# Optimization experiments

Measured on AMD Instinct MI355X. Metric: run time of the kernel, lower is better.

The kernel has to match this reference:

```python
import jax, jax.numpy as jnp
import numpy as np

K = 40  # k_point

def lrelu(v):
    return jax.nn.leaky_relu(v, 0.2)

def graph_feature(x, k):
    # x: [B, C, N] -> edge features [B, 2C, N, k] = concat(x_j - x_i, x_i)
    xx = jnp.sum(x * x, axis=1)                          # [B,N]
    inner = jnp.einsum('bcn,bcm->bnm', x, x)             # [B,N,N]
    dist = 2.0 * inner - xx[:, :, None] - xx[:, None, :] # negative squared distance
    idx = jax.lax.top_k(dist, k)[1]                      # [B,N,k] nearest neighbors
    xt = jnp.transpose(x, (0, 2, 1))                     # [B,N,C]
    nbr = jax.vmap(lambda f, i: f[i])(xt, idx)           # [B,N,k,C] gather
    ctr = xt[:, :, None, :]
    feat = jnp.concatenate([nbr - ctr, jnp.broadcast_to(ctr, nbr.shape)], axis=-1)
    return jnp.transpose(feat, (0, 3, 1, 2))             # [B,2C,N,k]

def conv2(f, w):  # 1x1 conv2d, no bias
    return jnp.einsum('bcnk,oc->bonk', f, w)

def conv1(f, w):  # 1x1 conv1d, no bias
    return jnp.einsum('bcn,oc->bon', f, w)

def edge_block(x, ws, k):
    f = graph_feature(x, k)
    for w in ws:
        f = lrelu(conv2(f, w))
    return jnp.max(f, axis=-1)                           # max over k neighbors

def setup_inputs() -> dict:
    key = jax.random.key(0)
    ks = jax.random.split(key, 20)
    B, N, NCLS, NSEG, D = 8, 2048, 16, 50, 1024
    def w(kk, o, c, s=0.05):
        return jax.random.normal(kk, (o, c), jnp.float32) * s
    return {
        'x': jax.random.normal(ks[0], (B, 3, N), jnp.float32),
        'l': jax.random.uniform(ks[1], (B, NCLS), dtype=jnp.float32),
        't_c1': w(ks[2], 64, 6), 't_c2': w(ks[3], 128, 64), 't_c3': w(ks[4], 1024, 128),
        't_f1': w(ks[5], 512, 1024), 't_f2': w(ks[6], 256, 512),
        't_f3_w': w(ks[7], 9, 256, 0.01),
        't_f3_b': jnp.eye(3, dtype=jnp.float32).reshape(9),  # identity-transform init
        'b1a': w(ks[8], 64, 6), 'b1b': w(ks[9], 64, 64),
        'b2a': w(ks[10], 64, 128), 'b2b': w(ks[11], 64, 64),
        'b3a': w(ks[12], 64, 128),
        'm1': w(ks[13], D, 192), 'm2': w(ks[14], 64, NCLS),
        'h1': w(ks[15], 256, D + 256), 'h2': w(ks[16], 256, 256),
        'h3': w(ks[17], 128, 256), 'h4': w(ks[18], NSEG, 128),
    }

def reference(x, l, t_c1, t_c2, t_c3, t_f1, t_f2, t_f3_w, t_f3_b,
              b1a, b1b, b2a, b2b, b3a, m1, m2, h1, h2, h3, h4):
    B, _, N = x.shape
    # transform net on graph features of raw points
    x0 = graph_feature(x, K)                              # [B,6,N,K]
    t = lrelu(conv2(x0, t_c1))
    t = lrelu(conv2(t, t_c2))
    t = jnp.max(t, axis=-1)                               # [B,128,N]
    t = lrelu(conv1(t, t_c3))
    t = jnp.max(t, axis=-1)                               # [B,1024]
    t = lrelu(t @ t_f1.T)
    t = lrelu(t @ t_f2.T)
    T = (t @ t_f3_w.T + t_f3_b).reshape(B, 3, 3)
    x = jnp.einsum('bji,bjn->bin', T, x)                  # T^T @ x
    # edge-conv blocks
    x1 = edge_block(x, [b1a, b1b], K)                     # [B,64,N]
    x2 = edge_block(x1, [b2a, b2b], K)                    # [B,64,N]
    x3 = edge_block(x2, [b3a], K)                         # [B,64,N]
    cat = jnp.concatenate([x1, x2, x3], axis=1)           # [B,192,N]
    g = jnp.max(lrelu(conv1(cat, m1)), axis=-1, keepdims=True)  # [B,1024,1]
    lv = lrelu(jnp.einsum('bc,oc->bo', l, m2))[:, :, None]      # [B,64,1]
    glob = jnp.broadcast_to(jnp.concatenate([g, lv], axis=1), (B, g.shape[1] + 64, N))
    h = jnp.concatenate([glob, x1, x2, x3], axis=1)       # [B,1280,N]
    h = lrelu(conv1(h, h1))
    h = lrelu(conv1(h, h2))
    h = lrelu(conv1(h, h3))
    return conv1(h, h4)                                   # [B,50,N]
```

## Files before the change

### kernel.cpp

```cpp
#include <hip/hip_runtime.h>
#include <cstdint>

#define NPTS 2048
#define BATCH 8
#define KNN 40

__device__ __forceinline__ float lrelu(float v){ return fmaxf(v, 0.2f*v); }
__device__ __forceinline__ bool better(float v1,int i1,float v2,int i2){
  return (v1>v2) || (v1==v2 && i1<i2);
}
__device__ __forceinline__ float4 ld4(const float* p){ return *(const float4*)p; }

#define INSERT8(v,id,d,m) \
  if (better(d, m, v[7], id[7])){ \
    v[7]=d; id[7]=m; \
    { if (better(v[7],id[7],v[6],id[6])){ float tv=v[6];int ti=id[6]; v[6]=v[7];id[6]=id[7]; v[7]=tv;id[7]=ti; } } \
    { if (better(v[6],id[6],v[5],id[5])){ float tv=v[5];int ti=id[5]; v[5]=v[6];id[5]=id[6]; v[6]=tv;id[6]=ti; } } \
    { if (better(v[5],id[5],v[4],id[4])){ float tv=v[4];int ti=id[4]; v[4]=v[5];id[4]=id[5]; v[5]=tv;id[5]=ti; } } \
    { if (better(v[4],id[4],v[3],id[3])){ float tv=v[3];int ti=id[3]; v[3]=v[4];id[3]=id[4]; v[4]=tv;id[4]=ti; } } \
    { if (better(v[3],id[3],v[2],id[2])){ float tv=v[2];int ti=id[2]; v[2]=v[3];id[2]=id[3]; v[3]=tv;id[3]=ti; } } \
    { if (better(v[2],id[2],v[1],id[1])){ float tv=v[1];int ti=id[1]; v[1]=v[2];id[1]=id[2]; v[2]=tv;id[2]=ti; } } \
    { if (better(v[1],id[1],v[0],id[0])){ float tv=v[0];int ti=id[0]; v[0]=v[1];id[0]=id[1]; v[1]=tv;id[1]=ti; } } \
  }

__global__ void transpose_kernel(const float* __restrict__ src, float* __restrict__ dst,
                                 int R, int C, int ld, int off){
  int i = blockIdx.x*256 + threadIdx.x;
  if (i < R*C){ int r = i / C, c = i % C; dst[c*R + r] = src[r*ld + off + c]; }
}

template<int TAG>
__global__ void norms_rows_kernel(const float* __restrict__ x, float* __restrict__ xx, int N){
  int b = blockIdx.y; int n = blockIdx.x*256 + threadIdx.x;
  const float* xb = x + (size_t)b*3*N;
  float v0 = xb[n], v1 = xb[N+n], v2 = xb[2*N+n];
  xx[(size_t)b*N + n] = v0*v0 + v1*v1 + v2*v2;
}

template<int TAG>
__global__ void norms_cl_kernel(const float* __restrict__ f, int off, float* __restrict__ xx, int N){
  int b = blockIdx.y; int n = blockIdx.x*256 + threadIdx.x;
  const float4* p = (const float4*)(f + ((size_t)b*N + n)*192 + off);
  float s = 0.f;
#pragma unroll
  for (int q=0;q<16;q++){ float4 v = p[q]; s += v.x*v.x + v.y*v.y + v.z*v.z + v.w*v.w; }
  xx[(size_t)b*N + n] = s;
}

__device__ __forceinline__ void sort8(float (&v)[8], int (&id)[8]){
#define CE(a,bq) { if (better(v[bq],id[bq],v[a],id[a])){ float tv=v[a]; int ti=id[a]; v[a]=v[bq]; id[a]=id[bq]; v[bq]=tv; id[bq]=ti; } }
  CE(0,1) CE(2,3) CE(4,5) CE(6,7)
  CE(0,2) CE(1,3) CE(4,6) CE(5,7)
  CE(1,2) CE(5,6)
  CE(0,4) CE(1,5) CE(2,6) CE(3,7)
  CE(2,4) CE(3,5)
  CE(1,2) CE(3,4) CE(5,6)
#undef CE
}

template<int TAG>
__global__ __launch_bounds__(256) void knn3_kernel(
    const float* __restrict__ xrows, const float* __restrict__ xx,
    int* __restrict__ idxT, int N){
  const int b = blockIdx.y, tid = threadIdx.x;
  const int w = tid>>6, lane = tid&63;
  const int nq = blockIdx.x*4 + w;
  const float* xb = xrows + (size_t)b*3*N;
  const float* xxb = xx + (size_t)b*N;
  float c0 = xb[nq], c1 = xb[N+nq], c2 = xb[2*N+nq];
  float xxn = xxb[nq];
  float v[8]; int id[8];
#pragma unroll
  for (int j=0;j<8;j++){ v[j]=-__builtin_inff(); id[j]=0x7FFFFFFF; }
  for (int j=0;j<32;j++){
    int m = j*64 + lane;
    float s = c0*xb[m] + c1*xb[N+m] + c2*xb[2*N+m];
    float d = 2.f*s - xxn - xxb[m];
    INSERT8(v, id, d, m)
  }
  float lastv = 0.f; int lasti = 0;
  int win = 0;
  for (int r=0;r<KNN;r++){
    float bv = v[0]; int bi = id[0];
#pragma unroll
    for (int off=32; off; off>>=1){
      float ov = __shfl_xor(bv, off);
      int   oi = __shfl_xor(bi, off);
      if (better(ov, oi, bv, bi)){ bv = ov; bi = oi; }
    }
    if (lane == r) win = bi;
    if (id[0] == bi){
      lastv = v[0]; lasti = id[0];
#pragma unroll
      for (int j=0;j<7;j++){ v[j]=v[j+1]; id[j]=id[j+1]; }
      v[7] = -__builtin_inff(); id[7] = 0x7FFFFFFF;
      if (id[0] == 0x7FFFFFFF){
        float nv = -__builtin_inff(); int ni = 0x7FFFFFFF;
        for (int j=0;j<32;j++){
          int m = j*64 + lane;
          float s = c0*xb[m] + c1*xb[N+m] + c2*xb[2*N+m];
          float dd = 2.f*s - xxn - xxb[m];
          if (better(lastv, lasti, dd, m) && better(dd, m, nv, ni)){ nv=dd; ni=m; }
        }
        v[0] = nv; id[0] = ni;
      }
    }
  }
  if (lane < KNN) idxT[((size_t)b*KNN + lane)*N + nq] = win;
}

template<int TAG>
__global__ __launch_bounds__(256) void knn64_kernel(
    const float* __restrict__ featT, int featOff,
    const float* __restrict__ xx, int* __restrict__ idxT, int N){
  const int b = blockIdx.y, tid = threadIdx.x;
  const int w = tid>>6, lane = tid&63;
  __shared__ float cand[32*64];
  __shared__ float dist[4*2048];
  const float* fb = featT + featOff;
  const float* xxb = xx + (size_t)b*N;
  const int nq = blockIdx.x*4 + w;
  const int h = lane>>5;
  float4 ctr8[8];
  {
    const float4* cp = (const float4*)(fb + ((size_t)b*N + nq)*192);
#pragma unroll
    for (int q=0;q<8;q++) ctr8[q] = cp[h*8 + q];
  }
  float xxn = xxb[nq];
  float* dw = &dist[w*2048];
  float4 g[2];
#pragma unroll
  for (int r=0;r<2;r++){
    int k2 = tid + 256*r;
    int c = k2>>4, f = k2&15;
    g[r] = ld4(&fb[((size_t)b*N + c)*192 + 4*f]);
  }
  const int cc = lane&31, swz = cc&15, qb = h*8;
  for (int t=0;t<64;t++){
    __syncthreads();
#pragma unroll
    for (int r=0;r<2;r++){
      int k2 = tid + 256*r;
      int c = k2>>4, f = k2&15;
      *(float4*)&cand[(c<<6) + ((f ^ (c&15))<<2)] = g[r];
    }
    __syncthreads();
    if (t+1 < 64){
      int m0n = (t+1)*32;
#pragma unroll
      for (int r=0;r<2;r++){
        int k2 = tid + 256*r;
        int c = k2>>4, f = k2&15;
        g[r] = ld4(&fb[((size_t)b*N + m0n + c)*192 + 4*f]);
      }
    }
    float s0=0.f,s1=0.f,s2=0.f,s3=0.f;
#pragma unroll
    for (int j=0;j<8;j++){
      float4 mv = *(const float4*)&cand[(cc<<6) + (((qb + j) ^ swz)<<2)];
      s0 = fmaf(ctr8[j].x, mv.x, s0);
      s1 = fmaf(ctr8[j].y, mv.y, s1);
      s2 = fmaf(ctr8[j].z, mv.z, s2);
      s3 = fmaf(ctr8[j].w, mv.w, s3);
    }
    float p = (s0+s1)+(s2+s3);
    float tot = p + __shfl_xor(p, 32);
    if (h == (t&1)){
      int m = t*32 + cc;
      dw[(t>>1)*64 + lane] = 2.f*tot - xxn - xxb[m];
    }
  }
  float v[8]; int id[8];
#pragma unroll
  for (int j=0;j<8;j++){ v[j]=dw[j*64+lane]; id[j]=j*64+lane; }
  sort8(v, id);
#pragma unroll
  for (int gq=1; gq<4; gq++){
    float a[8]; int ai[8];
#pragma unroll
    for (int j=0;j<8;j++){ a[j]=dw[(gq*8+j)*64+lane]; ai[j]=(gq*8+j)*64+lane; }
    sort8(a, ai);
    float m_[8]; int mi_[8];
#pragma unroll
    for (int k=0;k<8;k++){
      if (better(a[7-k], ai[7-k], v[k], id[k])){ m_[k]=a[7-k]; mi_[k]=ai[7-k]; }
      else                                     { m_[k]=v[k];   mi_[k]=id[k]; }
    }
#define CEB(x,y) { if (better(m_[y],mi_[y],m_[x],mi_[x])){ float tv=m_[x];int ti=mi_[x]; m_[x]=m_[y];mi_[x]=mi_[y]; m_[y]=tv;mi_[y]=ti; } }
    CEB(0,4) CEB(1,5) CEB(2,6) CEB(3,7)
    CEB(0,2) CEB(1,3) CEB(4,6) CEB(5,7)
    CEB(0,1) CEB(2,3) CEB(4,5) CEB(6,7)
#undef CEB
#pragma unroll
    for (int k=0;k<8;k++){ v[k]=m_[k]; id[k]=mi_[k]; }
  }
  float lastv = 0.f; int lasti = 0;
  int win = 0;
  for (int r=0;r<KNN;r++){
    float bv = v[0]; int bi = id[0];
#pragma unroll
    for (int off=32; off; off>>=1){
      float ov = __shfl_xor(bv, off);
      int   oi = __shfl_xor(bi, off);
      if (better(ov, oi, bv, bi)){ bv = ov; bi = oi; }
    }
    if (lane == r) win = bi;
    if (id[0] == bi){
      lastv = v[0]; lasti = id[0];
#pragma unroll
      for (int j=0;j<7;j++){ v[j]=v[j+1]; id[j]=id[j+1]; }
      v[7] = -__builtin_inff(); id[7] = 0x7FFFFFFF;
      if (id[0] == 0x7FFFFFFF){
        float nv = -__builtin_inff(); int ni = 0x7FFFFFFF;
        for (int j=0;j<32;j++){
          float vv = dw[j*64 + lane]; int m = j*64 + lane;
          if (better(lastv, lasti, vv, m) && better(vv, m, nv, ni)){ nv=vv; ni=m; }
        }
        v[0] = nv; id[0] = ni;
      }
    }
  }
  if (lane < KNN) idxT[((size_t)b*KNN + lane)*N + nq] = win;
}


__global__ __launch_bounds__(256) void edgeA_kernel(
    const float* __restrict__ x, const int* __restrict__ idxT,
    const float* __restrict__ w1, const float* __restrict__ w2,
    float* __restrict__ tT, int N){
  __shared__ float w1aT[3*64];
  __shared__ float wd3T[3*64];
  __shared__ float w2T[64*128];
  __shared__ float aT3[4][3*16];
  __shared__ float s1T[4][64*16];
  const int tid = threadIdx.x, w = tid>>6, lane = tid&63;
  const int oq = lane&7, rg = lane>>3;
  const int o0 = oq*8, r0 = rg*2;
  const int b = blockIdx.y, n0 = blockIdx.x*16;
  for (int i=tid; i<192; i+=256){
    int o = i&63, c = i/64;
    float a = w1[o*6+c];
    w1aT[c*64+o] = a; wd3T[c*64+o] = w1[o*6+3+c] - a;
  }
  for (int i=tid; i<128*64; i+=256){
    int o = i>>6, c = i&63;
    w2T[c*128+o] = w2[o*64+c];
  }
  if (tid < 48){ int c = tid>>4, r = tid&15; aT3[0][c*16+r] = x[((size_t)b*3+c)*N + n0 + r]; }
  __syncthreads();
  float base[16];
#pragma unroll
  for (int i=0;i<16;i++) base[i]=0.f;
#pragma unroll
  for (int c=0;c<3;c++){
    float4 wA = ld4(&wd3T[c*64+o0]), wB = ld4(&wd3T[c*64+o0+4]);
    float2 av = *(const float2*)&aT3[0][c*16+r0];
    float wv[8] = {wA.x,wA.y,wA.z,wA.w,wB.x,wB.y,wB.z,wB.w};
    float rv[2] = {av.x,av.y};
#pragma unroll
    for (int oo=0;oo<8;oo++)
#pragma unroll
      for (int rr=0;rr<2;rr++) base[oo*2+rr] = fmaf(wv[oo], rv[rr], base[oo*2+rr]);
  }
  __syncthreads();
  float mx[32];
#pragma unroll
  for (int i=0;i<32;i++) mx[i] = -__builtin_inff();
  for (int it=0; it<10; it++){
    int k = it*4 + w;
    int m = idxT[((size_t)b*KNN + k)*N + n0 + (lane&15)];
    if (lane < 48){ int c = lane>>4; aT3[w][c*16 + (lane&15)] = x[((size_t)b*3+c)*N + m]; }
    float acc[16];
#pragma unroll
    for (int i=0;i<16;i++) acc[i] = base[i];
#pragma unroll
    for (int c=0;c<3;c++){
      float4 wA = ld4(&w1aT[c*64+o0]), wB = ld4(&w1aT[c*64+o0+4]);
      float2 av = *(const float2*)&aT3[w][c*16+r0];
      float wv[8] = {wA.x,wA.y,wA.z,wA.w,wB.x,wB.y,wB.z,wB.w};
      float rv[2] = {av.x,av.y};
#pragma unroll
      for (int oo=0;oo<8;oo++)
#pragma unroll
        for (int rr=0;rr<2;rr++) acc[oo*2+rr] = fmaf(wv[oo], rv[rr], acc[oo*2+rr]);
    }
#pragma unroll
    for (int oo=0;oo<8;oo++){
      float2 sv; sv.x = lrelu(acc[oo*2]); sv.y = lrelu(acc[oo*2+1]);
      *(float2*)&s1T[w][(o0+oo)*16 + r0] = sv;
    }
    float acc2[32];
#pragma unroll
    for (int i=0;i<32;i++) acc2[i]=0.f;
    for (int c=0;c<64;c++){
      float2 av = *(const float2*)&s1T[w][c*16 + r0];
#pragma unroll
      for (int p=0;p<4;p++){
        float4 wv = ld4(&w2T[c*128 + p*32 + oq*4]);
        acc2[p*8+0] = fmaf(wv.x, av.x, acc2[p*8+0]);
        acc2[p*8+1] = fmaf(wv.x, av.y, acc2[p*8+1]);
        acc2[p*8+2] = fmaf(wv.y, av.x, acc2[p*8+2]);
        acc2[p*8+3] = fmaf(wv.y, av.y, acc2[p*8+3]);
        acc2[p*8+4] = fmaf(wv.z, av.x, acc2[p*8+4]);
        acc2[p*8+5] = fmaf(wv.z, av.y, acc2[p*8+5]);
        acc2[p*8+6] = fmaf(wv.w, av.x, acc2[p*8+6]);
        acc2[p*8+7] = fmaf(wv.w, av.y, acc2[p*8+7]);
      }
    }
#pragma unroll
    for (int i=0;i<32;i++) mx[i] = fmaxf(mx[i], lrelu(acc2[i]));
  }
  __syncthreads();
#pragma unroll
  for (int rr=0;rr<2;rr++){
#pragma unroll
    for (int p=0;p<4;p++){
      float4 a = make_float4(mx[p*8+0+rr], mx[p*8+2+rr], mx[p*8+4+rr], mx[p*8+6+rr]);
      *(float4*)&w2T[w*2048 + (r0+rr)*128 + p*32 + oq*4] = a;
    }
  }
  __syncthreads();
  for (int i=tid; i<2048; i+=256){
    float vv = fmaxf(fmaxf(w2T[i], w2T[2048+i]), fmaxf(w2T[4096+i], w2T[6144+i]));
    int r = i>>7, o = i&127;
    tT[((size_t)b*N + n0 + r)*128 + o] = vv;
  }
}

__global__ __launch_bounds__(128) void edgeB_kernel(
    const float* __restrict__ xp, const int* __restrict__ idxT,
    const float* __restrict__ w1, const float* __restrict__ w2,
    float* __restrict__ catT, int N){
  __shared__ float w1aT[3*64];
  __shared__ float wd3T[3*64];
  __shared__ float w2T[64*64];
  __shared__ float aT3[2][3*32];
  __shared__ float s1T[2][64*32];
  const int tid = threadIdx.x, w = tid>>6, lane = tid&63;
  const int oq = lane&7, rg = lane>>3;
  const int o0 = oq*8, r0 = rg*4;
  const int b = blockIdx.y, n0 = blockIdx.x*32;
  for (int i=tid; i<192; i+=128){
    int o = i&63, c = i>>6;
    float a = w1[o*6+c], bb = w1[o*6+3+c];
    w1aT[c*64+o] = a; wd3T[c*64+o] = bb - a;
  }
  for (int i=tid; i<64*64; i+=128){
    int o = i>>6, c = i&63;
    w2T[c*64+o] = w2[o*64+c];
  }
  if (tid < 32){
#pragma unroll
    for (int c=0;c<3;c++) aT3[0][c*32+tid] = xp[((size_t)b*3+c)*N + n0 + tid];
  }
  __syncthreads();
  float base[32];
#pragma unroll
  for (int i=0;i<32;i++) base[i]=0.f;
#pragma unroll
  for (int c=0;c<3;c++){
    float4 w0 = ld4(&wd3T[c*64+o0]), w1v = ld4(&wd3T[c*64+o0+4]);
    float4 av = ld4(&aT3[0][c*32+r0]);
    float wv[8] = {w0.x,w0.y,w0.z,w0.w,w1v.x,w1v.y,w1v.z,w1v.w};
    float rv[4] = {av.x,av.y,av.z,av.w};
#pragma unroll
    for (int oo=0;oo<8;oo++)
#pragma unroll
      for (int rr=0;rr<4;rr++) base[oo*4+rr] = fmaf(wv[oo], rv[rr], base[oo*4+rr]);
  }
  __syncthreads();
  float mx[32];
#pragma unroll
  for (int i=0;i<32;i++) mx[i] = -__builtin_inff();
  for (int it=0; it<20; it++){
    int k = it*2 + w;
    {
      int row = lane&31;
      int m = idxT[((size_t)b*KNN + k)*N + n0 + row];
      if (lane < 32){
#pragma unroll
        for (int c=0;c<3;c++) aT3[w][c*32+row] = xp[((size_t)b*3+c)*N + m];
      }
    }
    float acc[32];
#pragma unroll
    for (int i=0;i<32;i++) acc[i] = base[i];
#pragma unroll
    for (int c=0;c<3;c++){
      float4 w0 = ld4(&w1aT[c*64+o0]), w1v = ld4(&w1aT[c*64+o0+4]);
      float4 av = ld4(&aT3[w][c*32+r0]);
      float wv[8] = {w0.x,w0.y,w0.z,w0.w,w1v.x,w1v.y,w1v.z,w1v.w};
      float rv[4] = {av.x,av.y,av.z,av.w};
#pragma unroll
      for (int oo=0;oo<8;oo++)
#pragma unroll
        for (int rr=0;rr<4;rr++) acc[oo*4+rr] = fmaf(wv[oo], rv[rr], acc[oo*4+rr]);
    }
#pragma unroll
    for (int oo=0;oo<8;oo++){
      float4 sv = make_float4(lrelu(acc[oo*4+0]), lrelu(acc[oo*4+1]), lrelu(acc[oo*4+2]), lrelu(acc[oo*4+3]));
      *(float4*)&s1T[w][(o0+oo)*32 + r0] = sv;
    }
    float acc2[32];
#pragma unroll
    for (int i=0;i<32;i++) acc2[i]=0.f;
    for (int c=0;c<64;c++){
      float4 w0 = ld4(&w2T[c*64+o0]), w1v = ld4(&w2T[c*64+o0+4]);
      float4 av = ld4(&s1T[w][c*32+r0]);
      float wv[8] = {w0.x,w0.y,w0.z,w0.w,w1v.x,w1v.y,w1v.z,w1v.w};
      float rv[4] = {av.x,av.y,av.z,av.w};
#pragma unroll
      for (int oo=0;oo<8;oo++)
#pragma unroll
        for (int rr=0;rr<4;rr++) acc2[oo*4+rr] = fmaf(wv[oo], rv[rr], acc2[oo*4+rr]);
    }
#pragma unroll
    for (int i=0;i<32;i++) mx[i] = fmaxf(mx[i], lrelu(acc2[i]));
  }
  __syncthreads();
#pragma unroll
  for (int rr=0;rr<4;rr++){
    float4 a = make_float4(mx[0*4+rr], mx[1*4+rr], mx[2*4+rr], mx[3*4+rr]);
    float4 bq = make_float4(mx[4*4+rr], mx[5*4+rr], mx[6*4+rr], mx[7*4+rr]);
    *(float4*)&s1T[w][(r0+rr)*64 + o0] = a;
    *(float4*)&s1T[w][(r0+rr)*64 + o0 + 4] = bq;
  }
  __syncthreads();
  for (int i=tid; i<2048; i+=128){
    float v = fmaxf(s1T[0][i], s1T[1][i]);
    int r = i>>6, o = i&63;
    catT[((size_t)b*N + n0 + r)*192 + o] = v;
  }
}

__global__ __launch_bounds__(128) void edgeC_kernel(
    const float* __restrict__ inT, int inOff, const int* __restrict__ idxT,
    const float* __restrict__ w1, const float* __restrict__ w2,
    float* __restrict__ catT, int outOff, int N){
  __shared__ float w1T[64*64];
  __shared__ float w2T[64*64];
  __shared__ float aT[2][64*32];
  __shared__ float s1T[2][64*32];
  const int tid = threadIdx.x, w = tid>>6, lane = tid&63;
  const int oq = lane&7, rg = lane>>3;
  const int o0 = oq*8, r0 = rg*4;
  const int b = blockIdx.y, n0 = blockIdx.x*32;
  for (int i=tid; i<64*64; i+=128){
    int o = i>>6, c = i&63;
    float a = w1[o*128+c], bb = w1[o*128+64+c];
    w1T[c*64+o] = a; w2T[c*64+o] = bb - a;
  }
  for (int i=tid; i<512; i+=128){
    int p = i>>4, cq = i&15;
    float4 v = ld4(&inT[((size_t)b*N + n0 + p)*192 + inOff + cq*4]);
    aT[0][(cq*4+0)*32+p] = v.x; aT[0][(cq*4+1)*32+p] = v.y;
    aT[0][(cq*4+2)*32+p] = v.z; aT[0][(cq*4+3)*32+p] = v.w;
  }
  __syncthreads();
  float base[32];
#pragma unroll
  for (int i=0;i<32;i++) base[i]=0.f;
  for (int c=0;c<64;c++){
    float4 w0 = ld4(&w2T[c*64+o0]), w1v = ld4(&w2T[c*64+o0+4]);
    float4 av = ld4(&aT[0][c*32+r0]);
    float wv[8] = {w0.x,w0.y,w0.z,w0.w,w1v.x,w1v.y,w1v.z,w1v.w};
    float rv[4] = {av.x,av.y,av.z,av.w};
#pragma unroll
    for (int oo=0;oo<8;oo++)
#pragma unroll
      for (int rr=0;rr<4;rr++) base[oo*4+rr] = fmaf(wv[oo], rv[rr], base[oo*4+rr]);
  }
  __syncthreads();
  for (int i=tid; i<64*64; i+=128){
    int o = i>>6, c = i&63;
    w2T[c*64+o] = w2[o*64+c];
  }
  __syncthreads();
  float mx[32];
#pragma unroll
  for (int i=0;i<32;i++) mx[i] = -__builtin_inff();
  const int row = lane&31, ch = lane>>5;
  for (int it=0; it<20; it++){
    int k = it*2 + w;
    {
      int m = idxT[((size_t)b*KNN + k)*N + n0 + row];
      const float* src = &inT[((size_t)b*N + m)*192 + inOff + ch*32];
      float4 g[8];
#pragma unroll
      for (int j=0;j<8;j++) g[j] = ld4(src + j*4);
#pragma unroll
      for (int j=0;j<8;j++){
        aT[w][(ch*32+j*4+0)*32 + row] = g[j].x;
        aT[w][(ch*32+j*4+1)*32 + row] = g[j].y;
        aT[w][(ch*32+j*4+2)*32 + row] = g[j].z;
        aT[w][(ch*32+j*4+3)*32 + row] = g[j].w;
      }
    }
    float acc[32];
#pragma unroll
    for (int i=0;i<32;i++) acc[i] = base[i];
    for (int c=0;c<64;c++){
      float4 w0 = ld4(&w1T[c*64+o0]), w1v = ld4(&w1T[c*64+o0+4]);
      float4 av = ld4(&aT[w][c*32+r0]);
      float wv[8] = {w0.x,w0.y,w0.z,w0.w,w1v.x,w1v.y,w1v.z,w1v.w};
      float rv[4] = {av.x,av.y,av.z,av.w};
#pragma unroll
      for (int oo=0;oo<8;oo++)
#pragma unroll
        for (int rr=0;rr<4;rr++) acc[oo*4+rr] = fmaf(wv[oo], rv[rr], acc[oo*4+rr]);
    }
#pragma unroll
    for (int oo=0;oo<8;oo++){
      float4 sv = make_float4(lrelu(acc[oo*4+0]), lrelu(acc[oo*4+1]), lrelu(acc[oo*4+2]), lrelu(acc[oo*4+3]));
      *(float4*)&s1T[w][(o0+oo)*32 + r0] = sv;
    }
    float acc2[32];
#pragma unroll
    for (int i=0;i<32;i++) acc2[i]=0.f;
    for (int c=0;c<64;c++){
      float4 w0 = ld4(&w2T[c*64+o0]), w1v = ld4(&w2T[c*64+o0+4]);
      float4 av = ld4(&s1T[w][c*32+r0]);
      float wv[8] = {w0.x,w0.y,w0.z,w0.w,w1v.x,w1v.y,w1v.z,w1v.w};
      float rv[4] = {av.x,av.y,av.z,av.w};
#pragma unroll
      for (int oo=0;oo<8;oo++)
#pragma unroll
        for (int rr=0;rr<4;rr++) acc2[oo*4+rr] = fmaf(wv[oo], rv[rr], acc2[oo*4+rr]);
    }
#pragma unroll
    for (int i=0;i<32;i++) mx[i] = fmaxf(mx[i], lrelu(acc2[i]));
  }
  __syncthreads();
#pragma unroll
  for (int rr=0;rr<4;rr++){
    float4 a = make_float4(mx[0*4+rr], mx[1*4+rr], mx[2*4+rr], mx[3*4+rr]);
    float4 bq = make_float4(mx[4*4+rr], mx[5*4+rr], mx[6*4+rr], mx[7*4+rr]);
    *(float4*)&s1T[w][(r0+rr)*64 + o0] = a;
    *(float4*)&s1T[w][(r0+rr)*64 + o0 + 4] = bq;
  }
  __syncthreads();
  for (int i=tid; i<2048; i+=128){
    float v = fmaxf(s1T[0][i], s1T[1][i]);
    int r = i>>6, o = i&63;
    catT[((size_t)b*N + n0 + r)*192 + outOff + o] = v;
  }
}

__global__ __launch_bounds__(128) void edgeD_kernel(
    const float* __restrict__ inT, int inOff, const int* __restrict__ idxT,
    const float* __restrict__ w1, float* __restrict__ catT, int outOff, int N){
  __shared__ float w1T[64*64];
  __shared__ float wdT[64*64];
  __shared__ float aT[2][64*32];
  const int tid = threadIdx.x, w = tid>>6, lane = tid&63;
  const int oq = lane&7, rg = lane>>3;
  const int o0 = oq*8, r0 = rg*4;
  const int b = blockIdx.y, n0 = blockIdx.x*32;
  for (int i=tid; i<64*64; i+=128){
    int o = i>>6, c = i&63;
    float a = w1[o*128+c], bb = w1[o*128+64+c];
    w1T[c*64+o] = a; wdT[c*64+o] = bb - a;
  }
  for (int i=tid; i<512; i+=128){
    int p = i>>4, cq = i&15;
    float4 v = ld4(&inT[((size_t)b*N + n0 + p)*192 + inOff + cq*4]);
    aT[0][(cq*4+0)*32+p] = v.x; aT[0][(cq*4+1)*32+p] = v.y;
    aT[0][(cq*4+2)*32+p] = v.z; aT[0][(cq*4+3)*32+p] = v.w;
  }
  __syncthreads();
  float base[32];
#pragma unroll
  for (int i=0;i<32;i++) base[i]=0.f;
  for (int c=0;c<64;c++){
    float4 w0 = ld4(&wdT[c*64+o0]), w1v = ld4(&wdT[c*64+o0+4]);
    float4 av = ld4(&aT[0][c*32+r0]);
    float wv[8] = {w0.x,w0.y,w0.z,w0.w,w1v.x,w1v.y,w1v.z,w1v.w};
    float rv[4] = {av.x,av.y,av.z,av.w};
#pragma unroll
    for (int oo=0;oo<8;oo++)
#pragma unroll
      for (int rr=0;rr<4;rr++) base[oo*4+rr] = fmaf(wv[oo], rv[rr], base[oo*4+rr]);
  }
  __syncthreads();
  float mx[32];
#pragma unroll
  for (int i=0;i<32;i++) mx[i] = -__builtin_inff();
  const int row = lane&31, ch = lane>>5;
  for (int it=0; it<20; it++){
    int k = it*2 + w;
    {
      int m = idxT[((size_t)b*KNN + k)*N + n0 + row];
      const float* src = &inT[((size_t)b*N + m)*192 + inOff + ch*32];
      float4 g[8];
#pragma unroll
      for (int j=0;j<8;j++) g[j] = ld4(src + j*4);
#pragma unroll
      for (int j=0;j<8;j++){
        aT[w][(ch*32+j*4+0)*32 + row] = g[j].x;
        aT[w][(ch*32+j*4+1)*32 + row] = g[j].y;
        aT[w][(ch*32+j*4+2)*32 + row] = g[j].z;
        aT[w][(ch*32+j*4+3)*32 + row] = g[j].w;
      }
    }
    float acc[32];
#pragma unroll
    for (int i=0;i<32;i++) acc[i] = base[i];
    for (int c=0;c<64;c++){
      float4 w0 = ld4(&w1T[c*64+o0]), w1v = ld4(&w1T[c*64+o0+4]);
      float4 av = ld4(&aT[w][c*32+r0]);
      float wv[8] = {w0.x,w0.y,w0.z,w0.w,w1v.x,w1v.y,w1v.z,w1v.w};
      float rv[4] = {av.x,av.y,av.z,av.w};
#pragma unroll
      for (int oo=0;oo<8;oo++)
#pragma unroll
        for (int rr=0;rr<4;rr++) acc[oo*4+rr] = fmaf(wv[oo], rv[rr], acc[oo*4+rr]);
    }
#pragma unroll
    for (int i=0;i<32;i++) mx[i] = fmaxf(mx[i], lrelu(acc[i]));
  }
  __syncthreads();
#pragma unroll
  for (int rr=0;rr<4;rr++){
    float4 a = make_float4(mx[0*4+rr], mx[1*4+rr], mx[2*4+rr], mx[3*4+rr]);
    float4 bq = make_float4(mx[4*4+rr], mx[5*4+rr], mx[6*4+rr], mx[7*4+rr]);
    *(float4*)&wdT[w*2048 + (r0+rr)*64 + o0] = a;
    *(float4*)&wdT[w*2048 + (r0+rr)*64 + o0 + 4] = bq;
  }
  __syncthreads();
  for (int i=tid; i<2048; i+=128){
    float v = fmaxf(wdT[i], wdT[2048+i]);
    int r = i>>6, o = i&63;
    catT[((size_t)b*N + n0 + r)*192 + outOff + o] = v;
  }
}

template<int CIN, int TAG>
__global__ __launch_bounds__(128) void convmax_kernel(
    const float* __restrict__ inT, const float* __restrict__ wT,
    float* __restrict__ partial, int N){
  __shared__ float wsh[CIN*64];
  __shared__ float ish[32*CIN];
  const int tid = threadIdx.x, w = tid>>6, lane = tid&63;
  const int oq = lane&7, rg = lane>>3;
  const int o0 = oq*8;
  const int b = blockIdx.z, oc = blockIdx.x, nt = blockIdx.y;
  for (int i=tid; i<CIN*64; i+=128){
    int c = i>>6, o = i&63;
    wsh[i] = wT[(size_t)c*1024 + oc*64 + o];
  }
  float mx[32];
#pragma unroll
  for (int i=0;i<32;i++) mx[i] = -__builtin_inff();
  const int nbase = nt*(N/8);
  for (int st=0; st<8; st++){
    __syncthreads();
    const float* src = inT + ((size_t)b*N + nbase + st*32)*CIN;
    for (int i=tid; i<32*(CIN/4); i+=128){
      int p = i/(CIN/4), cq = i%(CIN/4);
      float4 v = ld4(src + p*CIN + 4*cq);
      int base = (((p>>2) ^ (cq&7))<<2) + (p&3);
      ish[(4*cq+0)*32 + base] = v.x;
      ish[(4*cq+1)*32 + base] = v.y;
      ish[(4*cq+2)*32 + base] = v.z;
      ish[(4*cq+3)*32 + base] = v.w;
    }
    __syncthreads();
    float acc[32];
#pragma unroll
    for (int i=0;i<32;i++) acc[i]=0.f;
    for (int c=0;c<CIN;c++){
      float4 w0 = ld4(&wsh[c*64+o0]), w1v = ld4(&wsh[c*64+o0+4]);
      float4 av = ld4(&ish[c*32 + ((rg ^ ((c>>2)&7))<<2)]);
      float wv[8] = {w0.x,w0.y,w0.z,w0.w,w1v.x,w1v.y,w1v.z,w1v.w};
      float rv[4] = {av.x,av.y,av.z,av.w};
#pragma unroll
      for (int oo=0;oo<8;oo++)
#pragma unroll
        for (int rr=0;rr<4;rr++) acc[oo*4+rr] = fmaf(wv[oo], rv[rr], acc[oo*4+rr]);
    }
#pragma unroll
    for (int i=0;i<32;i++) mx[i] = fmaxf(mx[i], lrelu(acc[i]));
  }
  float m8[8];
#pragma unroll
  for (int oo=0;oo<8;oo++)
    m8[oo] = fmaxf(fmaxf(mx[oo*4+0], mx[oo*4+1]), fmaxf(mx[oo*4+2], mx[oo*4+3]));
  __syncthreads();
  *(float4*)&ish[(w*8+rg)*64 + o0]     = make_float4(m8[0],m8[1],m8[2],m8[3]);
  *(float4*)&ish[(w*8+rg)*64 + o0 + 4] = make_float4(m8[4],m8[5],m8[6],m8[7]);
  __syncthreads();
  if (tid < 64){
    float v = -__builtin_inff();
#pragma unroll
    for (int g=0; g<16; g++) v = fmaxf(v, ish[g*64+tid]);
    partial[((size_t)b*8 + nt)*1024 + oc*64 + tid] = v;
  }
}

template<int TAG>
__global__ void reduce_max_kernel(const float* __restrict__ partial, float* __restrict__ out){
  int b = blockIdx.y; int o = blockIdx.x*256 + threadIdx.x;
  float v = -__builtin_inff();
  for (int s=0;s<8;s++) v = fmaxf(v, partial[((size_t)b*8 + s)*1024 + o]);
  out[(size_t)b*1024 + o] = v;
}

__global__ void fc_kernel(const float* __restrict__ in, const float* __restrict__ W,
                          const float* __restrict__ bias, float* __restrict__ out,
                          int CI, int O, int act){
  int b = blockIdx.x;
  __shared__ float insh[1024];
  for (int i=threadIdx.x;i<CI;i+=blockDim.x) insh[i]=in[(size_t)b*CI+i];
  __syncthreads();
  for (int o=threadIdx.x;o<O;o+=blockDim.x){
    float s = bias ? bias[o] : 0.f;
    for (int c=0;c<CI;c++) s = fmaf(W[(size_t)o*CI+c], insh[c], s);
    if (act) s = lrelu(s);
    out[(size_t)b*O+o]=s;
  }
}

__global__ void transform_kernel(const float* __restrict__ x, const float* __restrict__ T9,
                                 float* __restrict__ xp, int N){
  int b = blockIdx.y; int n = blockIdx.x*256 + threadIdx.x;
  const float* t = T9 + (size_t)b*9;
  float x0=x[((size_t)b*3+0)*N+n], x1=x[((size_t)b*3+1)*N+n], x2=x[((size_t)b*3+2)*N+n];
#pragma unroll
  for (int i=0;i<3;i++)
    xp[((size_t)b*3+i)*N+n] = t[i]*x0 + t[3+i]*x1 + t[6+i]*x2;
}

__global__ void bias1_kernel(const float* __restrict__ g, const float* __restrict__ lv,
                             const float* __restrict__ h1w, float* __restrict__ bias1){
  int b = blockIdx.x;
  __shared__ float insh[1088];
  for (int i=threadIdx.x;i<1088;i+=256) insh[i] = (i<1024)? g[(size_t)b*1024+i] : lv[(size_t)b*64 + (i-1024)];
  __syncthreads();
  int o = threadIdx.x;
  float s=0.f;
  for (int c=0;c<1088;c++) s = fmaf(h1w[(size_t)o*1280+c], insh[c], s);
  bias1[(size_t)b*256+o]=s;
}

template<int CI, int O, bool ACT>
__global__ __launch_bounds__(256) void conv1_kernel(
    const float* __restrict__ inT, const float* __restrict__ wT,
    const float* __restrict__ bias, float* __restrict__ outT, int N){
  const int b = blockIdx.y, n0 = blockIdx.x*32;
  __shared__ float insh[32*CI];
  const float* src = inT + ((size_t)b*N + n0)*CI;
  for (int i=threadIdx.x;i<32*CI;i+=256) insh[i] = src[i];
  __syncthreads();
  constexpr int NREP = 256/O;
  constexpr int NLOC = 32/NREP;
  const int o = threadIdx.x % O, rep = threadIdx.x / O;
  float acc[NLOC];
#pragma unroll
  for (int t=0;t<NLOC;t++) acc[t]=0.f;
  for (int c=0;c<CI;c++){
    float wv = wT[c*O + o];
#pragma unroll
    for (int t=0;t<NLOC;t++) acc[t] = fmaf(wv, insh[(t*NREP+rep)*CI + c], acc[t]);
  }
  float bv = bias ? bias[(size_t)b*O + o] : 0.f;
#pragma unroll
  for (int t=0;t<NLOC;t++){
    float s = acc[t] + bv;
    if (ACT) s = lrelu(s);
    outT[((size_t)b*N + n0 + t*NREP + rep)*O + o] = s;
  }
}

__global__ __launch_bounds__(256) void conv_out_kernel(
    const float* __restrict__ inT, const float* __restrict__ wT,
    float* __restrict__ out, int N){
  const int b = blockIdx.y, n0 = blockIdx.x*32;
  __shared__ float insh[32*129];
  const float* src = inT + ((size_t)b*N + n0)*128;
  for (int i=threadIdx.x;i<32*128;i+=256){ int nn=i>>7, c=i&127; insh[nn*129+c]=src[i]; }
  __syncthreads();
  const int nl = threadIdx.x & 31, og = threadIdx.x >> 5;
  float acc[7];
#pragma unroll
  for (int t=0;t<7;t++) acc[t]=0.f;
  for (int c=0;c<128;c++){
    float iv = insh[nl*129+c];
#pragma unroll
    for (int t=0;t<7;t++){
      int o = og + 8*t;
      float wv = (o<50)? wT[c*50+o] : 0.f;
      acc[t] = fmaf(wv, iv, acc[t]);
    }
  }
#pragma unroll
  for (int t=0;t<7;t++){
    int o = og + 8*t;
    if (o < 50) out[((size_t)b*50+o)*N + n0 + nl] = acc[t];
  }
}

extern "C" void kernel_launch(void* const* d_in, const int* in_sizes, int n_in,
                              void* d_out, int out_size, void* d_ws, size_t ws_size,
                              hipStream_t stream){
  const float* x    = (const float*)d_in[0];
  const float* l    = (const float*)d_in[1];
  const float* t_c1 = (const float*)d_in[2];
  const float* t_c2 = (const float*)d_in[3];
  const float* t_c3 = (const float*)d_in[4];
  const float* t_f1 = (const float*)d_in[5];
  const float* t_f2 = (const float*)d_in[6];
  const float* t_f3w= (const float*)d_in[7];
  const float* t_f3b= (const float*)d_in[8];
  const float* b1a  = (const float*)d_in[9];
  const float* b1b  = (const float*)d_in[10];
  const float* b2a  = (const float*)d_in[11];
  const float* b2b  = (const float*)d_in[12];
  const float* b3a  = (const float*)d_in[13];
  const float* m1   = (const float*)d_in[14];
  const float* m2   = (const float*)d_in[15];
  const float* h1   = (const float*)d_in[16];
  const float* h2   = (const float*)d_in[17];
  const float* h3   = (const float*)d_in[18];
  const float* h4   = (const float*)d_in[19];
  float* out = (float*)d_out;
  float* ws = (float*)d_ws;
  const int N = NPTS, B = BATCH;

  size_t off = 0;
  auto alloc = [&](size_t nf){ float* p = ws + off; off += nf; return p; };
  float* WT_TC3 = alloc((size_t)128*1024);
  float* WT_M1  = alloc((size_t)192*1024);
  float* WT_H1B = alloc((size_t)192*256);
  float* WT_H2  = alloc((size_t)256*256);
  float* WT_H3  = alloc((size_t)256*128);
  float* WT_H4  = alloc((size_t)128*64);
  int*   IDXT   = (int*)alloc((size_t)B*N*KNN);
  float* XX     = alloc((size_t)B*N);
  float* TT     = alloc((size_t)B*N*128);
  float* PARTIAL= alloc((size_t)B*8*1024);
  float* TG     = alloc((size_t)B*1024);
  float* T512   = alloc((size_t)B*512);
  float* T256   = alloc((size_t)B*256);
  float* T9     = alloc((size_t)B*16);
  float* XP     = alloc((size_t)B*3*N);
  float* CATT   = alloc((size_t)B*N*192);
  float* G      = alloc((size_t)B*1024);
  float* LV     = alloc((size_t)B*64);
  float* BIAS1  = alloc((size_t)B*256);
  float* H1T    = alloc((size_t)B*N*256);
  float* H2T    = alloc((size_t)B*N*256);
  float* H3T    = alloc((size_t)B*N*128);
  (void)ws_size; (void)in_sizes; (void)n_in; (void)out_size;

  dim3 blk(256);
  dim3 eblk(128);
  transpose_kernel<<<dim3((1024*128+255)/256), blk, 0, stream>>>(t_c3, WT_TC3, 1024,128,128,0);
  transpose_kernel<<<dim3((1024*192+255)/256), blk, 0, stream>>>(m1,  WT_M1, 1024,192,192,0);
  transpose_kernel<<<dim3((256*192+255)/256),  blk, 0, stream>>>(h1, WT_H1B, 256,192,1280,1088);
  transpose_kernel<<<dim3((256*256+255)/256),  blk, 0, stream>>>(h2, WT_H2, 256,256,256,0);
  transpose_kernel<<<dim3((128*256+255)/256),  blk, 0, stream>>>(h3, WT_H3, 128,256,256,0);
  transpose_kernel<<<dim3((50*128+255)/256),   blk, 0, stream>>>(h4, WT_H4, 50,128,128,0);

  norms_rows_kernel<0><<<dim3(N/256,B), blk, 0, stream>>>(x, XX, N);
  knn3_kernel<0><<<dim3(N/4,B), blk, 0, stream>>>(x, XX, IDXT, N);
  edgeA_kernel<<<dim3(N/16,B), blk, 0, stream>>>(x, IDXT, t_c1, t_c2, TT, N);
  convmax_kernel<128,0><<<dim3(16,8,B), eblk, 0, stream>>>(TT, WT_TC3, PARTIAL, N);
  reduce_max_kernel<0><<<dim3(4,B), blk, 0, stream>>>(PARTIAL, TG);
  fc_kernel<<<dim3(B), dim3(512), 0, stream>>>(TG, t_f1, nullptr, T512, 1024, 512, 1);
  fc_kernel<<<dim3(B), dim3(512), 0, stream>>>(T512, t_f2, nullptr, T256, 512, 256, 1);
  fc_kernel<<<dim3(B), dim3(512), 0, stream>>>(T256, t_f3w, t_f3b, T9, 256, 9, 0);
  transform_kernel<<<dim3(N/256,B), blk, 0, stream>>>(x, T9, XP, N);

  norms_rows_kernel<1><<<dim3(N/256,B), blk, 0, stream>>>(XP, XX, N);
  knn3_kernel<1><<<dim3(N/4,B), blk, 0, stream>>>(XP, XX, IDXT, N);
  edgeB_kernel<<<dim3(N/32,B), eblk, 0, stream>>>(XP, IDXT, b1a, b1b, CATT, N);

  norms_cl_kernel<0><<<dim3(N/256,B), blk, 0, stream>>>(CATT, 0, XX, N);
  knn64_kernel<0><<<dim3(N/4,B), blk, 0, stream>>>(CATT, 0, XX, IDXT, N);
  edgeC_kernel<<<dim3(N/32,B), eblk, 0, stream>>>(CATT, 0, IDXT, b2a, b2b, CATT, 64, N);

  norms_cl_kernel<1><<<dim3(N/256,B), blk, 0, stream>>>(CATT, 64, XX, N);
  knn64_kernel<1><<<dim3(N/4,B), blk, 0, stream>>>(CATT, 64, XX, IDXT, N);
  edgeD_kernel<<<dim3(N/32,B), eblk, 0, stream>>>(CATT, 64, IDXT, b3a, CATT, 128, N);

  convmax_kernel<192,1><<<dim3(16,8,B), eblk, 0, stream>>>(CATT, WT_M1, PARTIAL, N);
  reduce_max_kernel<1><<<dim3(4,B), blk, 0, stream>>>(PARTIAL, G);
  fc_kernel<<<dim3(B), dim3(512), 0, stream>>>(l, m2, nullptr, LV, 16, 64, 1);
  bias1_kernel<<<dim3(B), blk, 0, stream>>>(G, LV, h1, BIAS1);
  conv1_kernel<192,256,true><<<dim3(N/32,B), blk, 0, stream>>>(CATT, WT_H1B, BIAS1, H1T, N);
  conv1_kernel<256,256,true><<<dim3(N/32,B), blk, 0, stream>>>(H1T, WT_H2, nullptr, H2T, N);
  conv1_kernel<256,128,true><<<dim3(N/32,B), blk, 0, stream>>>(H2T, WT_H3, nullptr, H3T, N);
  conv_out_kernel<<<dim3(N/32,B), blk, 0, stream>>>(H3T, WT_H4, out, N);
}
```

Before: 2.384 ms.

## Register-tile head convs over output channels and split convmax staging per wave

The head conv1 kernels are rewritten as register-tiled GEMMs. Each thread computes 8 outputs by 2 points, weights and inputs are staged in LDS in channel chunks, and the output channels are split across a third grid dimension. This replaces the old one-output-per-thread loop that read weights from global memory. The convmax kernel gives each wave its own input buffer and alternating point tiles, which removes the block-wide barriers inside the loop. The cost is more blocks that each reload input tiles, plus extra LDS use.

```diff
diff --git a/kernel.cpp b/kernel.cpp
--- a/kernel.cpp
+++ b/kernel.cpp
@@ -640,38 +640,39 @@
     const float* __restrict__ inT, const float* __restrict__ wT,
     float* __restrict__ partial, int N){
   __shared__ float wsh[CIN*64];
-  __shared__ float ish[32*CIN];
+  __shared__ float ish[2][32*CIN];
   const int tid = threadIdx.x, w = tid>>6, lane = tid&63;
   const int oq = lane&7, rg = lane>>3;
-  const int o0 = oq*8;
+  const int o0 = oq*8, r0 = rg*4;
   const int b = blockIdx.z, oc = blockIdx.x, nt = blockIdx.y;
   for (int i=tid; i<CIN*64; i+=128){
     int c = i>>6, o = i&63;
     wsh[i] = wT[(size_t)c*1024 + oc*64 + o];
   }
+  __syncthreads();
   float mx[32];
 #pragma unroll
   for (int i=0;i<32;i++) mx[i] = -__builtin_inff();
   const int nbase = nt*(N/8);
-  for (int st=0; st<8; st++){
-    __syncthreads();
+  float* mish = ish[w];
+  for (int it=0; it<4; it++){
+    const int st = it*2 + w;
     const float* src = inT + ((size_t)b*N + nbase + st*32)*CIN;
-    for (int i=tid; i<32*(CIN/4); i+=128){
+    for (int i=lane; i<32*(CIN/4); i+=64){
       int p = i/(CIN/4), cq = i%(CIN/4);
       float4 v = ld4(src + p*CIN + 4*cq);
       int base = (((p>>2) ^ (cq&7))<<2) + (p&3);
-      ish[(4*cq+0)*32 + base] = v.x;
-      ish[(4*cq+1)*32 + base] = v.y;
-      ish[(4*cq+2)*32 + base] = v.z;
-      ish[(4*cq+3)*32 + base] = v.w;
-    }
-    __syncthreads();
+      mish[(4*cq+0)*32 + base] = v.x;
+      mish[(4*cq+1)*32 + base] = v.y;
+      mish[(4*cq+2)*32 + base] = v.z;
+      mish[(4*cq+3)*32 + base] = v.w;
+    }
     float acc[32];
 #pragma unroll
     for (int i=0;i<32;i++) acc[i]=0.f;
     for (int c=0;c<CIN;c++){
       float4 w0 = ld4(&wsh[c*64+o0]), w1v = ld4(&wsh[c*64+o0+4]);
-      float4 av = ld4(&ish[c*32 + ((rg ^ ((c>>2)&7))<<2)]);
+      float4 av = ld4(&mish[c*32 + ((rg ^ ((c>>2)&7))<<2)]);
       float wv[8] = {w0.x,w0.y,w0.z,w0.w,w1v.x,w1v.y,w1v.z,w1v.w};
       float rv[4] = {av.x,av.y,av.z,av.w};
 #pragma unroll
@@ -687,13 +688,14 @@
   for (int oo=0;oo<8;oo++)
     m8[oo] = fmaxf(fmaxf(mx[oo*4+0], mx[oo*4+1]), fmaxf(mx[oo*4+2], mx[oo*4+3]));
   __syncthreads();
-  *(float4*)&ish[(w*8+rg)*64 + o0]     = make_float4(m8[0],m8[1],m8[2],m8[3]);
-  *(float4*)&ish[(w*8+rg)*64 + o0 + 4] = make_float4(m8[4],m8[5],m8[6],m8[7]);
+  float* mb = ish[0];
+  *(float4*)&mb[(w*8+rg)*64 + o0]     = make_float4(m8[0],m8[1],m8[2],m8[3]);
+  *(float4*)&mb[(w*8+rg)*64 + o0 + 4] = make_float4(m8[4],m8[5],m8[6],m8[7]);
   __syncthreads();
   if (tid < 64){
     float v = -__builtin_inff();
 #pragma unroll
-    for (int g=0; g<16; g++) v = fmaxf(v, ish[g*64+tid]);
+    for (int g=0; g<16; g++) v = fmaxf(v, mb[g*64+tid]);
     partial[((size_t)b*8 + nt)*1024 + oc*64 + tid] = v;
   }
 }
@@ -744,31 +746,70 @@
 }
 
 template<int CI, int O, bool ACT>
-__global__ __launch_bounds__(256) void conv1_kernel(
+__global__ __launch_bounds__(128) void conv1_kernel(
     const float* __restrict__ inT, const float* __restrict__ wT,
     const float* __restrict__ bias, float* __restrict__ outT, int N){
-  const int b = blockIdx.y, n0 = blockIdx.x*32;
-  __shared__ float insh[32*CI];
+  constexpr int CCH = (CI % 128 == 0) ? 128 : 96;
+  constexpr int NCH = CI / CCH;
+  __shared__ float wsh[CCH*64];
+  __shared__ float ish[32*CCH];
+  const int tid = threadIdx.x, w = tid>>6, lane = tid&63;
+  const int oq = lane&7, rg = lane>>3;
+  const int o0 = oq*8, r0 = w*16 + rg*2;
+  const int b = blockIdx.y, n0 = blockIdx.x*32, oc = blockIdx.z;
   const float* src = inT + ((size_t)b*N + n0)*CI;
-  for (int i=threadIdx.x;i<32*CI;i+=256) insh[i] = src[i];
-  __syncthreads();
-  constexpr int NREP = 256/O;
-  constexpr int NLOC = 32/NREP;
-  const int o = threadIdx.x % O, rep = threadIdx.x / O;
-  float acc[NLOC];
-#pragma unroll
-  for (int t=0;t<NLOC;t++) acc[t]=0.f;
-  for (int c=0;c<CI;c++){
-    float wv = wT[c*O + o];
-#pragma unroll
-    for (int t=0;t<NLOC;t++) acc[t] = fmaf(wv, insh[(t*NREP+rep)*CI + c], acc[t]);
-  }
-  float bv = bias ? bias[(size_t)b*O + o] : 0.f;
-#pragma unroll
-  for (int t=0;t<NLOC;t++){
-    float s = acc[t] + bv;
-    if (ACT) s = lrelu(s);
-    outT[((size_t)b*N + n0 + t*NREP + rep)*O + o] = s;
+  float acc[16];
+#pragma unroll
+  for (int i=0;i<16;i++) acc[i]=0.f;
+  for (int ch=0; ch<NCH; ch++){
+    const int cc0 = ch*CCH;
+    if (ch) __syncthreads();
+    for (int i=tid; i<CCH*64; i+=128){
+      int c = i>>6, od = i&63;
+      wsh[i] = wT[(size_t)(cc0+c)*O + oc*64 + od];
+    }
+    for (int i=tid; i<32*(CCH/4); i+=128){
+      int p = i/(CCH/4), cq = i%(CCH/4);
+      float4 v = ld4(src + p*CI + cc0 + 4*cq);
+      int base = (((p>>2) ^ (cq&7))<<2) + (p&3);
+      ish[(4*cq+0)*32 + base] = v.x;
+      ish[(4*cq+1)*32 + base] = v.y;
+      ish[(4*cq+2)*32 + base] = v.z;
+      ish[(4*cq+3)*32 + base] = v.w;
+    }
+    __syncthreads();
+    for (int c=0;c<CCH;c++){
+      float4 w0 = ld4(&wsh[c*64+o0]), w1v = ld4(&wsh[c*64+o0+4]);
+      float2 av = *(const float2*)&ish[c*32 + ((((r0>>2) ^ ((c>>2)&7))<<2) + (r0&3))];
+      float wv[8] = {w0.x,w0.y,w0.z,w0.w,w1v.x,w1v.y,w1v.z,w1v.w};
+      float rv[2] = {av.x,av.y};
+#pragma unroll
+      for (int oo=0;oo<8;oo++)
+#pragma unroll
+        for (int rr=0;rr<2;rr++) acc[oo*2+rr] = fmaf(wv[oo], rv[rr], acc[oo*2+rr]);
+    }
+  }
+  float bv[8];
+  if (bias){
+    float4 b0 = ld4(&bias[(size_t)b*O + oc*64 + o0]);
+    float4 b1 = ld4(&bias[(size_t)b*O + oc*64 + o0 + 4]);
+    bv[0]=b0.x; bv[1]=b0.y; bv[2]=b0.z; bv[3]=b0.w;
+    bv[4]=b1.x; bv[5]=b1.y; bv[6]=b1.z; bv[7]=b1.w;
+  } else {
+#pragma unroll
+    for (int i=0;i<8;i++) bv[i]=0.f;
+  }
+#pragma unroll
+  for (int rr=0;rr<2;rr++){
+    float oa[8];
+#pragma unroll
+    for (int oo=0;oo<8;oo++){
+      float s = acc[oo*2+rr] + bv[oo];
+      oa[oo] = ACT ? lrelu(s) : s;
+    }
+    float* dst = &outT[((size_t)b*N + n0 + r0 + rr)*O + oc*64 + o0];
+    *(float4*)dst     = make_float4(oa[0],oa[1],oa[2],oa[3]);
+    *(float4*)(dst+4) = make_float4(oa[4],oa[5],oa[6],oa[7]);
   }
 }
 
@@ -888,8 +929,8 @@
   reduce_max_kernel<1><<<dim3(4,B), blk, 0, stream>>>(PARTIAL, G);
   fc_kernel<<<dim3(B), dim3(512), 0, stream>>>(l, m2, nullptr, LV, 16, 64, 1);
   bias1_kernel<<<dim3(B), blk, 0, stream>>>(G, LV, h1, BIAS1);
-  conv1_kernel<192,256,true><<<dim3(N/32,B), blk, 0, stream>>>(CATT, WT_H1B, BIAS1, H1T, N);
-  conv1_kernel<256,256,true><<<dim3(N/32,B), blk, 0, stream>>>(H1T, WT_H2, nullptr, H2T, N);
-  conv1_kernel<256,128,true><<<dim3(N/32,B), blk, 0, stream>>>(H2T, WT_H3, nullptr, H3T, N);
+  conv1_kernel<192,256,true><<<dim3(N/32,B,4), eblk, 0, stream>>>(CATT, WT_H1B, BIAS1, H1T, N);
+  conv1_kernel<256,256,true><<<dim3(N/32,B,4), eblk, 0, stream>>>(H1T, WT_H2, nullptr, H2T, N);
+  conv1_kernel<256,128,true><<<dim3(N/32,B,2), eblk, 0, stream>>>(H2T, WT_H3, nullptr, H3T, N);
   conv_out_kernel<<<dim3(N/32,B), blk, 0, stream>>>(H3T, WT_H4, out, N);
 }
```

Result: faster. 2.326 ms (-2.4%).
